# Kernel tuning notes

Hardware: AMD Instinct MI355X
Metric: run time of the kernel (lower is better)

Reference implementation:

```python
import jax, jax.numpy as jnp
import numpy as np

D_IN = 2048
D_OUT = 2048
NUM_HEADS = 16
HEAD_DIM = D_OUT // NUM_HEADS


def setup_inputs() -> dict:
    key = jax.random.key(0)
    ks = jax.random.split(key, 6)
    b, t = 2, 2048
    x = jax.random.normal(ks[0], (b, t, D_IN), dtype=jnp.float32)
    s = 0.02
    Wq = jax.random.normal(ks[1], (D_OUT, D_IN), dtype=jnp.float32) * s
    Wk = jax.random.normal(ks[2], (D_OUT, D_IN), dtype=jnp.float32) * s
    Wv = jax.random.normal(ks[3], (D_OUT, D_IN), dtype=jnp.float32) * s
    Wo = jax.random.normal(ks[4], (D_OUT, D_OUT), dtype=jnp.float32) * s
    bo = jnp.zeros((D_OUT,), dtype=jnp.float32)
    theta = (10000.0 ** (-jnp.arange(0, HEAD_DIM, 2, dtype=jnp.float32) / HEAD_DIM))
    return {"x": x, "Wq": Wq, "Wk": Wk, "Wv": Wv, "Wo": Wo, "bo": bo, "theta": theta}


def _rope(v, sin, cos):
    # v: [b, t, h, d]; split even/odd feature indices, rotate, concat halves
    ve, vo = v[..., ::2], v[..., 1::2]
    return jnp.concatenate([ve * cos - vo * sin, ve * sin + vo * cos], axis=-1)


def reference(x, Wq, Wk, Wv, Wo, bo, theta):
    b, t, _ = x.shape
    q = (x @ Wq.T).reshape(b, t, NUM_HEADS, HEAD_DIM)
    k = (x @ Wk.T).reshape(b, t, NUM_HEADS, HEAD_DIM)
    v = (x @ Wv.T).reshape(b, t, NUM_HEADS, HEAD_DIM)

    pos = jnp.arange(t, dtype=jnp.float32)[:, None]          # [t, 1]
    freq = pos * theta[None, :]                              # [t, d/2]
    sin = jnp.sin(freq)[None, :, None, :]                    # [1, t, 1, d/2]
    cos = jnp.cos(freq)[None, :, None, :]
    q = _rope(q, sin, cos)
    k = _rope(k, sin, cos)

    # [b, h, t, t]
    scores = jnp.einsum('bqhd,bkhd->bhqk', q, k)
    causal = jnp.triu(jnp.ones((t, t), dtype=bool), k=1)
    scores = jnp.where(causal[None, None], -jnp.inf, scores)
    attn = jax.nn.softmax(scores / jnp.sqrt(jnp.float32(HEAD_DIM)), axis=-1)

    ctx = jnp.einsum('bhqk,bkhd->bqhd', attn, v).reshape(b, t, D_OUT)
    return ctx @ Wo.T + bo
```

## Files before the change

kernel.cpp:

```cpp
#include <hip/hip_runtime.h>

typedef unsigned short ushortT;
typedef short short8 __attribute__((ext_vector_type(8)));
typedef float floatx4 __attribute__((ext_vector_type(4)));

#define D_MODEL 2048
#define HEAD_DIM 128
#define NUM_HEADS 16
#define SEQ 2048
#define BATCH 2
#define M_TOK (BATCH * SEQ)
#define QKV_ELEMS ((size_t)M_TOK * D_MODEL)
#define W_ELEMS ((size_t)D_MODEL * D_MODEL)

__device__ __forceinline__ float bf2f(ushortT h) {
    return __uint_as_float(((unsigned int)h) << 16);
}
__device__ __forceinline__ ushortT f2bf(float f) {
    unsigned int u = __float_as_uint(f);
    u = u + 0x7fffu + ((u >> 16) & 1u);
    return (ushortT)(u >> 16);
}

__device__ __forceinline__ void gload_lds16(const ushortT* g, short* lds_wave_base) {
    __builtin_amdgcn_global_load_lds(
        (const __attribute__((address_space(1))) unsigned int*)g,
        (__attribute__((address_space(3))) unsigned int*)lds_wave_base,
        16, 0, 0);
}

__global__ __launch_bounds__(256) void cvt_all(
    const float* __restrict__ x,  const float* __restrict__ wq,
    const float* __restrict__ wk, const float* __restrict__ wv,
    const float* __restrict__ wo,
    ushortT* __restrict__ xb,  ushortT* __restrict__ wqb,
    ushortT* __restrict__ wkb, ushortT* __restrict__ wvb,
    ushortT* __restrict__ wob)
{
    const size_t XC = QKV_ELEMS / 8;
    const size_t WC = W_ELEMS / 8;
    size_t c = (size_t)blockIdx.x * 256 + threadIdx.x;
    const float* s; ushortT* d;
    if (c < XC)              { s = x;  d = xb;  }
    else if ((c -= XC) < WC) { s = wq; d = wqb; }
    else if ((c -= WC) < WC) { s = wk; d = wkb; }
    else if ((c -= WC) < WC) { s = wv; d = wvb; }
    else     { c -= WC;        s = wo; d = wob; }
    const float* f = s + c * 8;
    floatx4 a = *(const floatx4*)f;
    floatx4 b = *(const floatx4*)(f + 4);
    short8 r;
    r[0] = (short)f2bf(a.x); r[1] = (short)f2bf(a.y);
    r[2] = (short)f2bf(a.z); r[3] = (short)f2bf(a.w);
    r[4] = (short)f2bf(b.x); r[5] = (short)f2bf(b.y);
    r[6] = (short)f2bf(b.z); r[7] = (short)f2bf(b.w);
    *(short8*)(d + c * 8) = r;
}

template<bool OUTF32, bool VFRAG>
__global__ __launch_bounds__(256) void gemm_bt(
    const ushortT* __restrict__ A,
    const ushortT* __restrict__ W0, const ushortT* __restrict__ W1,
    const ushortT* __restrict__ W2,
    void* C0, void* C1, void* C2, const float* __restrict__ bias)
{
    __shared__ short As[128 * 64];
    __shared__ short Bs[128 * 64];

    const int z = blockIdx.z;
    const ushortT* W = (z == 0) ? W0 : (z == 1 ? W1 : W2);
    void* C = (z == 0) ? C0 : (z == 1 ? C1 : C2);

    const int tid  = threadIdx.x;
    const int wave = tid >> 6;
    const int lane = tid & 63;
    const int lr   = lane & 15;
    const int quad = lane >> 4;
    const int wm   = (wave & 1) * 64;
    const int wn   = (wave >> 1) * 64;

    const int blockM = blockIdx.y * 128;
    const int blockN = blockIdx.x * 128;

    const int srow = tid >> 3;
    const int scol = (tid & 7) * 8;
    const int scolSwz = scol ^ ((srow & 7) << 3);
    const ushortT* ag = A + (size_t)(blockM + srow) * D_MODEL + scolSwz;
    const ushortT* wg = W + (size_t)(blockN + srow) * D_MODEL + scolSwz;
    short* al = As + wave * 512;
    short* bl = Bs + wave * 512;

    const int rswz = (lr & 7) << 3;

    floatx4 acc[4][4];
    #pragma unroll
    for (int i = 0; i < 4; i++)
        #pragma unroll
        for (int j = 0; j < 4; j++) acc[i][j] = (floatx4){0.f, 0.f, 0.f, 0.f};

    for (int kk = 0; kk < D_MODEL; kk += 64) {
        #pragma unroll
        for (int i = 0; i < 4; i++) {
            gload_lds16(ag + kk + (size_t)(i * 32) * D_MODEL, al + i * 2048);
            gload_lds16(wg + kk + (size_t)(i * 32) * D_MODEL, bl + i * 2048);
        }
        __syncthreads();

        #pragma unroll
        for (int kh = 0; kh < 2; kh++) {
            const int cbase = (kh * 32 + quad * 8) ^ rswz;
            short8 af[4], bf[4];
            #pragma unroll
            for (int s = 0; s < 4; s++) {
                af[s] = *(const short8*)&As[(wm + s * 16 + lr) * 64 + cbase];
                bf[s] = *(const short8*)&Bs[(wn + s * 16 + lr) * 64 + cbase];
            }
            #pragma unroll
            for (int sm = 0; sm < 4; sm++)
                #pragma unroll
                for (int sn = 0; sn < 4; sn++)
                    acc[sm][sn] = __builtin_amdgcn_mfma_f32_16x16x32_bf16(
                        af[sm], bf[sn], acc[sm][sn], 0, 0, 0);
        }
        __syncthreads();
    }

    #pragma unroll
    for (int sm = 0; sm < 4; sm++) {
        const int row0 = blockM + wm + sm * 16 + quad * 4;
        #pragma unroll
        for (int sn = 0; sn < 4; sn++) {
            const int col = blockN + wn + sn * 16 + lr;
            const float bval = bias ? bias[col] : 0.f;
            #pragma unroll
            for (int rr = 0; rr < 4; rr++) {
                const float val = acc[sm][sn][rr] + bval;
                const int row = row0 + rr;
                if (VFRAG && z == 2) {
                    const int tt = row & (SEQ - 1);
                    const int bh2 = ((row >> 11) << 4) | (col >> 7);
                    const int dd = col & 127;
                    const size_t idx =
                        ((size_t)(bh2 * 8 + (dd >> 4)) * 64 + (tt >> 5)) * 512 +
                        (size_t)((((tt & 31) >> 3) * 16 + (dd & 15)) * 8 + (tt & 7));
                    ((ushortT*)C)[idx] = f2bf(val);
                } else if constexpr (OUTF32) {
                    ((float*)C)[(size_t)row * D_MODEL + col] = val;
                } else {
                    ((ushortT*)C)[(size_t)row * D_MODEL + col] = f2bf(val);
                }
            }
        }
    }
}

__global__ __launch_bounds__(256) void kpack_kernel(
    const ushortT* __restrict__ k, ushortT* __restrict__ kf,
    const float* __restrict__ theta)
{
    const int kt16 = blockIdx.x;
    const int bh   = blockIdx.y;
    const int b = bh >> 4, h = bh & 15;
    const int tid = threadIdx.x;
    const int ks = tid >> 6, lane = tid & 63;
    const int lr = lane & 15, quad = lane >> 4;

    const int t   = kt16 * 16 + lr;
    const int d0  = ks * 32 + quad * 8;
    const int dd0 = d0 & 63;
    const ushortT* src = k + (size_t)(b * SEQ + t) * D_MODEL + h * HEAD_DIM;
    short8 a  = *(const short8*)(src + 2 * dd0);
    short8 b8 = *(const short8*)(src + 2 * dd0 + 8);
    const float tp = (float)t;

    short8 v;
    #pragma unroll
    for (int j = 0; j < 8; j++) {
        const float ve = bf2f((ushortT)(j < 4 ? a[2 * j]     : b8[2 * j - 8]));
        const float vo = bf2f((ushortT)(j < 4 ? a[2 * j + 1] : b8[2 * j - 7]));
        const float ang = tp * theta[dd0 + j];
        const float s = sinf(ang), c = cosf(ang);
        v[j] = (short)f2bf((d0 < 64) ? (ve * c - vo * s) : (ve * s + vo * c));
    }
    *(short8*)(kf + ((size_t)(bh * 128 + kt16) * 4 + ks) * 512 + lane * 8) = v;
}

__global__ __launch_bounds__(256) void flash_attn2(
    const ushortT* __restrict__ q, const ushortT* __restrict__ kf,
    const ushortT* __restrict__ vf, ushortT* __restrict__ ctx,
    const float* __restrict__ theta)
{
    __shared__ short Kt[2][16 * 512];
    __shared__ short Vt[2][16 * 512];
    __shared__ short Pl[4][16][72];

    const unsigned lid = blockIdx.x;
    const int xcd  = lid & 7;
    const int slot = lid >> 3;
    const int ih   = slot >> 4;
    const int qtb  = slot & 15;
    const int bh   = (ih << 3) | xcd;

    const int b = bh >> 4, h = bh & 15;
    const size_t base = (size_t)b * SEQ * D_MODEL + h * HEAD_DIM;
    const size_t kfb = (size_t)bh * 128 * 4 * 512;
    const size_t vfb = (size_t)bh * 8 * 64 * 512;
    const int tid = threadIdx.x;
    const int w = tid >> 6, lane = tid & 63;
    const int lr = lane & 15, quad = lane >> 4;
    short* myP = &Pl[w][0][0];

    short8 onesf;
    #pragma unroll
    for (int j = 0; j < 8; j++) onesf[j] = (short)0x3F80;

    auto stage_tile = [&](int kt0, int buf) {
        const ushortT* ksrc = kf + kfb + (size_t)kt0 * 128;
        #pragma unroll
        for (int c = 0; c < 4; c++)
            gload_lds16(ksrc + c * 2048 + tid * 8, &Kt[buf][c * 2048 + w * 512]);
        #pragma unroll
        for (int c = 0; c < 4; c++) {
            const int e    = c * 2048 + tid * 8;
            const int dsub = e >> 10;
            const int rem  = e & 1023;
            const ushortT* vsrc = vf + vfb +
                ((size_t)dsub * 64 + (kt0 >> 5) + (rem >> 9)) * 512 + (rem & 511);
            gload_lds16(vsrc, &Vt[buf][c * 2048 + w * 512]);
        }
    };

    for (int pass = 0; pass < 2; pass++) {
        const int qt = (pass == 0) ? qtb : (SEQ / 64 - 1 - qtb);
        const int q0 = qt * 64 + w * 16;

        short8 Qf[4];
        {
            const ushortT* qrow = q + base + (size_t)(q0 + lr) * D_MODEL;
            const float tp = (float)(q0 + lr);
            #pragma unroll
            for (int ks = 0; ks < 4; ks++) {
                const int d0  = ks * 32 + quad * 8;
                const int dd0 = d0 & 63;
                short8 a  = *(const short8*)(qrow + 2 * dd0);
                short8 b8 = *(const short8*)(qrow + 2 * dd0 + 8);
                #pragma unroll
                for (int j = 0; j < 8; j++) {
                    const float ve = bf2f((ushortT)(j < 4 ? a[2 * j]     : b8[2 * j - 8]));
                    const float vo = bf2f((ushortT)(j < 4 ? a[2 * j + 1] : b8[2 * j - 7]));
                    const float ang = tp * theta[dd0 + j];
                    const float s = sinf(ang), c = cosf(ang);
                    const float r = (d0 < 64) ? (ve * c - vo * s) : (ve * s + vo * c);
                    Qf[ks][j] = (short)f2bf(r * 0.08838834764831845f);
                }
            }
        }

        floatx4 Of[8];
        #pragma unroll
        for (int i = 0; i < 8; i++) Of[i] = (floatx4){0.f, 0.f, 0.f, 0.f};
        floatx4 lacc = (floatx4){0.f, 0.f, 0.f, 0.f};

        stage_tile(0, 0);
        asm volatile("s_waitcnt vmcnt(0)" ::: "memory");
        __builtin_amdgcn_s_barrier();
        asm volatile("" ::: "memory");

        const int ntiles = qt + 1;
        for (int t = 0; t < ntiles; ++t) {
            const int buf = t & 1;
            const int kt0 = t * 64;

            floatx4 Sf[4];
            #pragma unroll
            for (int sub = 0; sub < 4; sub++) {
                floatx4 acc = {0.f, 0.f, 0.f, 0.f};
                #pragma unroll
                for (int ks = 0; ks < 4; ks++) {
                    short8 Kf_ = *(const short8*)(&Kt[buf][(sub * 4 + ks) * 512 + lane * 8]);
                    acc = __builtin_amdgcn_mfma_f32_16x16x32_bf16(Qf[ks], Kf_, acc, 0, 0, 0);
                }
                Sf[sub] = acc;
            }

            if (kt0 == qt * 64) {
                #pragma unroll
                for (int sub = 0; sub < 4; sub++) {
                    const int ktg = kt0 + sub * 16 + lr;
                    #pragma unroll
                    for (int i = 0; i < 4; i++)
                        if (ktg > q0 + quad * 4 + i) Sf[sub][i] = -1e30f;
                }
            }

            #pragma unroll
            for (int sub = 0; sub < 4; sub++) {
                #pragma unroll
                for (int i = 0; i < 4; i++) {
                    const float p = __expf(fminf(Sf[sub][i], 60.f));
                    myP[(quad * 4 + i) * 72 + sub * 16 + lr] = (short)f2bf(p);
                }
            }

            short8 Vr[16];
            #pragma unroll
            for (int dsub = 0; dsub < 8; dsub++) {
                Vr[2 * dsub]     = *(const short8*)(&Vt[buf][dsub * 1024 + lane * 8]);
                Vr[2 * dsub + 1] = *(const short8*)(&Vt[buf][dsub * 1024 + 512 + lane * 8]);
            }

            if (t + 1 < ntiles) stage_tile((t + 1) * 64, buf ^ 1);

            asm volatile("s_waitcnt lgkmcnt(0)" ::: "memory");
            short8 Pf0 = *(const short8*)(myP + lr * 72 + quad * 8);
            short8 Pf1 = *(const short8*)(myP + lr * 72 + 32 + quad * 8);

            lacc = __builtin_amdgcn_mfma_f32_16x16x32_bf16(Pf0, onesf, lacc, 0, 0, 0);
            lacc = __builtin_amdgcn_mfma_f32_16x16x32_bf16(Pf1, onesf, lacc, 0, 0, 0);

            #pragma unroll
            for (int dsub = 0; dsub < 8; dsub++) {
                Of[dsub] = __builtin_amdgcn_mfma_f32_16x16x32_bf16(
                    Pf0, Vr[2 * dsub], Of[dsub], 0, 0, 0);
                Of[dsub] = __builtin_amdgcn_mfma_f32_16x16x32_bf16(
                    Pf1, Vr[2 * dsub + 1], Of[dsub], 0, 0, 0);
            }

            asm volatile("s_waitcnt vmcnt(0)" ::: "memory");
            __builtin_amdgcn_s_barrier();
            asm volatile("" ::: "memory");
        }

        float inv[4];
        #pragma unroll
        for (int i = 0; i < 4; i++) inv[i] = 1.f / lacc[i];
        #pragma unroll
        for (int dsub = 0; dsub < 8; dsub++)
            #pragma unroll
            for (int i = 0; i < 4; i++)
                ctx[base + (size_t)(q0 + quad * 4 + i) * D_MODEL + dsub * 16 + lr] =
                    f2bf(Of[dsub][i] * inv[i]);
    }
}

extern "C" void kernel_launch(void* const* d_in, const int* in_sizes, int n_in,
                              void* d_out, int out_size, void* d_ws, size_t ws_size,
                              hipStream_t stream) {
    const float* x     = (const float*)d_in[0];
    const float* Wq    = (const float*)d_in[1];
    const float* Wk    = (const float*)d_in[2];
    const float* Wv    = (const float*)d_in[3];
    const float* Wo    = (const float*)d_in[4];
    const float* bo    = (const float*)d_in[5];
    const float* theta = (const float*)d_in[6];

    ushortT* ws  = (ushortT*)d_ws;
    ushortT* qb   = ws;
    ushortT* kb   = ws + QKV_ELEMS;
    ushortT* vfb  = ws + 2 * QKV_ELEMS;
    ushortT* kfbp = ws + 3 * QKV_ELEMS;
    ushortT* xb   = kfbp;
    ushortT* wqb  = ws + 4 * QKV_ELEMS;
    ushortT* wkb  = wqb + W_ELEMS;
    ushortT* wvb  = wkb + W_ELEMS;
    ushortT* wob  = wvb + W_ELEMS;
    ushortT* ctx  = wqb;

    cvt_all<<<dim3((unsigned)((QKV_ELEMS / 8 + 4 * (W_ELEMS / 8)) / 256)), 256, 0, stream>>>(
        x, Wq, Wk, Wv, Wo, xb, wqb, wkb, wvb, wob);

    gemm_bt<false, true><<<dim3(D_MODEL / 128, M_TOK / 128, 3), 256, 0, stream>>>(
        xb, wqb, wkb, wvb, qb, kb, vfb, nullptr);

    kpack_kernel<<<dim3(SEQ / 16, BATCH * NUM_HEADS), 256, 0, stream>>>(kb, kfbp, theta);

    flash_attn2<<<dim3(512), 256, 0, stream>>>(qb, kfbp, vfb, ctx, theta);

    gemm_bt<true, false><<<dim3(D_MODEL / 128, M_TOK / 128, 1), 256, 0, stream>>>(
        ctx, wob, wob, wob, d_out, d_out, d_out, bo);
}
```

Baseline: 441.7 us.

## Precompute RoPE sin/cos table, shrink GEMM K-tile, vectorize V-fragment stores

Adds a kernel that builds a shared sin/cos table, which kpack and the attention Q-load now read instead of calling sinf/cosf per element. The GEMM K-tile drops from 64 to 32 and the XOR swizzle is removed, halving LDS use but doubling the number of barrier-separated iterations and possibly adding bank conflicts. The V-fragment epilogue now writes four bf16 values as one vector store instead of four scalar stores. The table is placed in the wvb workspace slot, which is free once the QKV GEMM has run.

```diff
diff --git a/kernel.cpp b/kernel.cpp
--- a/kernel.cpp
+++ b/kernel.cpp
@@ -2,6 +2,7 @@
 
 typedef unsigned short ushortT;
 typedef short short8 __attribute__((ext_vector_type(8)));
+typedef short short4v __attribute__((ext_vector_type(4)));
 typedef float floatx4 __attribute__((ext_vector_type(4)));
 
 #define D_MODEL 2048
@@ -57,6 +58,16 @@
     *(short8*)(d + c * 8) = r;
 }
 
+__global__ __launch_bounds__(256) void sincos_kernel(
+    float* __restrict__ tbl, const float* __restrict__ theta)
+{
+    const int p = blockIdx.x * 256 + threadIdx.x;
+    const int t = p >> 6, d = p & 63;
+    const float ang = (float)t * theta[d];
+    tbl[2 * p]     = sinf(ang);
+    tbl[2 * p + 1] = cosf(ang);
+}
+
 template<bool OUTF32, bool VFRAG>
 __global__ __launch_bounds__(256) void gemm_bt(
     const ushortT* __restrict__ A,
@@ -64,8 +75,8 @@
     const ushortT* __restrict__ W2,
     void* C0, void* C1, void* C2, const float* __restrict__ bias)
 {
-    __shared__ short As[128 * 64];
-    __shared__ short Bs[128 * 64];
+    __shared__ short As[128 * 32];
+    __shared__ short Bs[128 * 32];
 
     const int z = blockIdx.z;
     const ushortT* W = (z == 0) ? W0 : (z == 1 ? W1 : W2);
@@ -82,15 +93,12 @@
     const int blockM = blockIdx.y * 128;
     const int blockN = blockIdx.x * 128;
 
-    const int srow = tid >> 3;
-    const int scol = (tid & 7) * 8;
-    const int scolSwz = scol ^ ((srow & 7) << 3);
-    const ushortT* ag = A + (size_t)(blockM + srow) * D_MODEL + scolSwz;
-    const ushortT* wg = W + (size_t)(blockN + srow) * D_MODEL + scolSwz;
+    const int srow = tid >> 2;
+    const int scol = (tid & 3) * 8;
+    const ushortT* ag = A + (size_t)(blockM + srow) * D_MODEL + scol;
+    const ushortT* wg = W + (size_t)(blockN + srow) * D_MODEL + scol;
     short* al = As + wave * 512;
     short* bl = Bs + wave * 512;
-
-    const int rswz = (lr & 7) << 3;
 
     floatx4 acc[4][4];
     #pragma unroll
@@ -98,30 +106,25 @@
         #pragma unroll
         for (int j = 0; j < 4; j++) acc[i][j] = (floatx4){0.f, 0.f, 0.f, 0.f};
 
-    for (int kk = 0; kk < D_MODEL; kk += 64) {
-        #pragma unroll
-        for (int i = 0; i < 4; i++) {
-            gload_lds16(ag + kk + (size_t)(i * 32) * D_MODEL, al + i * 2048);
-            gload_lds16(wg + kk + (size_t)(i * 32) * D_MODEL, bl + i * 2048);
-        }
+    for (int kk = 0; kk < D_MODEL; kk += 32) {
+        gload_lds16(ag + kk,                 al);
+        gload_lds16(ag + kk + 64 * D_MODEL,  al + 64 * 32);
+        gload_lds16(wg + kk,                 bl);
+        gload_lds16(wg + kk + 64 * D_MODEL,  bl + 64 * 32);
         __syncthreads();
 
-        #pragma unroll
-        for (int kh = 0; kh < 2; kh++) {
-            const int cbase = (kh * 32 + quad * 8) ^ rswz;
-            short8 af[4], bf[4];
-            #pragma unroll
-            for (int s = 0; s < 4; s++) {
-                af[s] = *(const short8*)&As[(wm + s * 16 + lr) * 64 + cbase];
-                bf[s] = *(const short8*)&Bs[(wn + s * 16 + lr) * 64 + cbase];
-            }
-            #pragma unroll
-            for (int sm = 0; sm < 4; sm++)
-                #pragma unroll
-                for (int sn = 0; sn < 4; sn++)
-                    acc[sm][sn] = __builtin_amdgcn_mfma_f32_16x16x32_bf16(
-                        af[sm], bf[sn], acc[sm][sn], 0, 0, 0);
-        }
+        short8 af[4], bf[4];
+        #pragma unroll
+        for (int s = 0; s < 4; s++) {
+            af[s] = *(const short8*)&As[(wm + s * 16 + lr) * 32 + quad * 8];
+            bf[s] = *(const short8*)&Bs[(wn + s * 16 + lr) * 32 + quad * 8];
+        }
+        #pragma unroll
+        for (int sm = 0; sm < 4; sm++)
+            #pragma unroll
+            for (int sn = 0; sn < 4; sn++)
+                acc[sm][sn] = __builtin_amdgcn_mfma_f32_16x16x32_bf16(
+                    af[sm], bf[sn], acc[sm][sn], 0, 0, 0);
         __syncthreads();
     }
 
@@ -132,22 +135,26 @@
         for (int sn = 0; sn < 4; sn++) {
             const int col = blockN + wn + sn * 16 + lr;
             const float bval = bias ? bias[col] : 0.f;
-            #pragma unroll
-            for (int rr = 0; rr < 4; rr++) {
-                const float val = acc[sm][sn][rr] + bval;
-                const int row = row0 + rr;
-                if (VFRAG && z == 2) {
-                    const int tt = row & (SEQ - 1);
-                    const int bh2 = ((row >> 11) << 4) | (col >> 7);
-                    const int dd = col & 127;
-                    const size_t idx =
-                        ((size_t)(bh2 * 8 + (dd >> 4)) * 64 + (tt >> 5)) * 512 +
-                        (size_t)((((tt & 31) >> 3) * 16 + (dd & 15)) * 8 + (tt & 7));
-                    ((ushortT*)C)[idx] = f2bf(val);
-                } else if constexpr (OUTF32) {
-                    ((float*)C)[(size_t)row * D_MODEL + col] = val;
-                } else {
-                    ((ushortT*)C)[(size_t)row * D_MODEL + col] = f2bf(val);
+            if (VFRAG && z == 2) {
+                const int tt0 = row0 & (SEQ - 1);
+                const int bh2 = ((row0 >> 11) << 4) | (col >> 7);
+                const int dd  = col & 127;
+                short4v v4;
+                #pragma unroll
+                for (int rr = 0; rr < 4; rr++)
+                    v4[rr] = (short)f2bf(acc[sm][sn][rr]);
+                const size_t idx0 =
+                    ((size_t)(bh2 * 8 + (dd >> 4)) * 64 + (tt0 >> 5)) * 512 +
+                    (size_t)((((tt0 & 31) >> 3) * 16 + (dd & 15)) * 8 + (tt0 & 7));
+                *(short4v*)((ushortT*)C + idx0) = v4;
+            } else {
+                #pragma unroll
+                for (int rr = 0; rr < 4; rr++) {
+                    const float val = acc[sm][sn][rr] + bval;
+                    if constexpr (OUTF32)
+                        ((float*)C)[(size_t)(row0 + rr) * D_MODEL + col] = val;
+                    else
+                        ((ushortT*)C)[(size_t)(row0 + rr) * D_MODEL + col] = f2bf(val);
                 }
             }
         }
@@ -156,7 +163,7 @@
 
 __global__ __launch_bounds__(256) void kpack_kernel(
     const ushortT* __restrict__ k, ushortT* __restrict__ kf,
-    const float* __restrict__ theta)
+    const float* __restrict__ tbl)
 {
     const int kt16 = blockIdx.x;
     const int bh   = blockIdx.y;
@@ -171,15 +178,14 @@
     const ushortT* src = k + (size_t)(b * SEQ + t) * D_MODEL + h * HEAD_DIM;
     short8 a  = *(const short8*)(src + 2 * dd0);
     short8 b8 = *(const short8*)(src + 2 * dd0 + 8);
-    const float tp = (float)t;
+    const float* tb = tbl + 2 * ((size_t)t * 64 + dd0);
 
     short8 v;
     #pragma unroll
     for (int j = 0; j < 8; j++) {
         const float ve = bf2f((ushortT)(j < 4 ? a[2 * j]     : b8[2 * j - 8]));
         const float vo = bf2f((ushortT)(j < 4 ? a[2 * j + 1] : b8[2 * j - 7]));
-        const float ang = tp * theta[dd0 + j];
-        const float s = sinf(ang), c = cosf(ang);
+        const float s = tb[2 * j], c = tb[2 * j + 1];
         v[j] = (short)f2bf((d0 < 64) ? (ve * c - vo * s) : (ve * s + vo * c));
     }
     *(short8*)(kf + ((size_t)(bh * 128 + kt16) * 4 + ks) * 512 + lane * 8) = v;
@@ -188,7 +194,7 @@
 __global__ __launch_bounds__(256) void flash_attn2(
     const ushortT* __restrict__ q, const ushortT* __restrict__ kf,
     const ushortT* __restrict__ vf, ushortT* __restrict__ ctx,
-    const float* __restrict__ theta)
+    const float* __restrict__ tbl)
 {
     __shared__ short Kt[2][16 * 512];
     __shared__ short Vt[2][16 * 512];
@@ -237,19 +243,19 @@
         short8 Qf[4];
         {
             const ushortT* qrow = q + base + (size_t)(q0 + lr) * D_MODEL;
-            const float tp = (float)(q0 + lr);
+            const float* trow = tbl + 2 * ((size_t)(q0 + lr) * 64);
             #pragma unroll
             for (int ks = 0; ks < 4; ks++) {
                 const int d0  = ks * 32 + quad * 8;
                 const int dd0 = d0 & 63;
                 short8 a  = *(const short8*)(qrow + 2 * dd0);
                 short8 b8 = *(const short8*)(qrow + 2 * dd0 + 8);
+                const float* tb = trow + 2 * dd0;
                 #pragma unroll
                 for (int j = 0; j < 8; j++) {
                     const float ve = bf2f((ushortT)(j < 4 ? a[2 * j]     : b8[2 * j - 8]));
                     const float vo = bf2f((ushortT)(j < 4 ? a[2 * j + 1] : b8[2 * j - 7]));
-                    const float ang = tp * theta[dd0 + j];
-                    const float s = sinf(ang), c = cosf(ang);
+                    const float s = tb[2 * j], c = tb[2 * j + 1];
                     const float r = (d0 < 64) ? (ve * c - vo * s) : (ve * s + vo * c);
                     Qf[ks][j] = (short)f2bf(r * 0.08838834764831845f);
                 }
@@ -365,6 +371,7 @@
     ushortT* wvb  = wkb + W_ELEMS;
     ushortT* wob  = wvb + W_ELEMS;
     ushortT* ctx  = wqb;
+    float*   tbl  = (float*)wvb;
 
     cvt_all<<<dim3((unsigned)((QKV_ELEMS / 8 + 4 * (W_ELEMS / 8)) / 256)), 256, 0, stream>>>(
         x, Wq, Wk, Wv, Wo, xb, wqb, wkb, wvb, wob);
@@ -372,9 +379,11 @@
     gemm_bt<false, true><<<dim3(D_MODEL / 128, M_TOK / 128, 3), 256, 0, stream>>>(
         xb, wqb, wkb, wvb, qb, kb, vfb, nullptr);
 
-    kpack_kernel<<<dim3(SEQ / 16, BATCH * NUM_HEADS), 256, 0, stream>>>(kb, kfbp, theta);
-
-    flash_attn2<<<dim3(512), 256, 0, stream>>>(qb, kfbp, vfb, ctx, theta);
+    sincos_kernel<<<dim3(SEQ * 64 / 256), 256, 0, stream>>>(tbl, theta);
+
+    kpack_kernel<<<dim3(SEQ / 16, BATCH * NUM_HEADS), 256, 0, stream>>>(kb, kfbp, tbl);
+
+    flash_attn2<<<dim3(512), 256, 0, stream>>>(qb, kfbp, vfb, ctx, tbl);
 
     gemm_bt<true, false><<<dim3(D_MODEL / 128, M_TOK / 128, 1), 256, 0, stream>>>(
         ctx, wob, wob, wob, d_out, d_out, d_out, bo);
```

Measured after the change: 412.7 us. 6.6% less time.
